# Kernel tuning notes

Measured on AMD Instinct MI355X. Metric: run time of the kernel, lower is better.

## Reference

```python
import jax, jax.numpy as jnp
import numpy as np
import math

B, D, NSTEPS = 16384, 256, 5
TEMP, ALPHA, ALPHA_A, ETA, EPS = 2.0, 0.2, 0.5, 1.0e4, 1e-10


def setup_inputs() -> dict:
    key = jax.random.key(0)
    ks = jax.random.split(key, 7)
    x = jax.random.bernoulli(ks[0], 0.5, (B, D)).astype(jnp.float32)  # binary state
    x_a = jax.random.normal(ks[1], (B, D), jnp.float32)  # auxiliary (continuous)
    A = jax.random.normal(ks[2], (D, D), jnp.float32)
    W = 0.1 * (A + A.T) / math.sqrt(D)  # symmetric coupling of quadratic EBM
    b = 0.1 * jax.random.normal(ks[3], (D,), jnp.float32)
    rr = jax.random.uniform(ks[4], (NSTEPS, B, D), jnp.float32)  # flip uniforms
    noise = jax.random.normal(ks[5], (NSTEPS, B, D), jnp.float32)  # Langevin noise
    accept_u = jax.random.uniform(ks[6], (NSTEPS, B), jnp.float32)  # MH uniforms
    return {"x": x, "x_a": x_a, "W": W, "b": b, "rr": rr, "noise": noise, "accept_u": accept_u}


def reference(x, x_a, W, b, rr, noise, accept_u):
    term2 = 1.0 / (2.0 * ALPHA)

    def energy(z):  # model(z): quadratic EBM, [B]
        return 0.5 * jnp.einsum('bd,de,be->b', z, W, z) + z @ b

    def diff_fn(z):  # approx_difference_function / temp: grad_E(z) * -(2z-1) / temp
        return (z @ W + b) * -(2.0 * z - 1.0) / TEMP

    def agrad(z, za):  # auxillary_gradient_function(eta, z, za)
        return (z - za) / ETA

    def step(carry, inp):
        x_cur, x_a_cur = carry
        rr_i, noise_i, u_i = inp
        ga = agrad(x_cur, x_a_cur)
        gm = diff_fn(x_cur) - ga / TEMP * -(2.0 * x_cur - 1.0)
        # exp(t)/(exp(t)+1) == sigmoid(t)
        flip_prob = jax.nn.sigmoid(gm - term2)
        ind = (rr_i < flip_prob).astype(x_cur.dtype)
        x_delta = (1.0 - x_cur) * ind + x_cur * (1.0 - ind)
        x_delta_a = x_a_cur + 0.5 * ALPHA_A * ga + math.sqrt(ALPHA_A) * noise_i
        lp_forward = jnp.sum(jnp.log(flip_prob * ind + (1.0 - flip_prob) * (1.0 - ind) + EPS), axis=-1)
        ga2 = agrad(x_delta, x_delta_a)
        gm2 = diff_fn(x_delta) - ga2 / TEMP * -(2.0 * x_delta - 1.0)
        fp2 = jax.nn.sigmoid(gm2 - term2)
        lp_reverse = jnp.sum(jnp.log(fp2 * ind + (1.0 - fp2) * (1.0 - ind) + EPS), axis=-1)
        m_term = (energy(x_delta) - jnp.sum((x_delta - x_delta_a) ** 2, axis=1) / (2.0 * ETA)) \
               - (energy(x_cur) - jnp.sum((x_cur - x_a_cur) ** 2, axis=1) / (2.0 * ETA))
        add_rev = jnp.sum((x_a_cur - (x_delta_a + 0.5 * ALPHA_A * ga2)) ** 2, axis=1) / (-2.0 * ALPHA_A)
        add_fwd = jnp.sum((x_delta_a - (x_a_cur + 0.5 * ALPHA_A * ga)) ** 2, axis=1) / (-2.0 * ALPHA_A)
        la = m_term + add_rev - add_fwd + lp_reverse - lp_forward
        # exp(la) > u  <=>  la > log(u); avoids overflow of exp
        a = (la > jnp.log(u_i)).astype(x_cur.dtype)
        x_new = x_delta * a[:, None] + x_cur * (1.0 - a[:, None])
        xa_new = x_delta_a * a[:, None] + x_a_cur * (1.0 - a[:, None])
        return (x_new, xa_new), None

    (x_out, xa_out), _ = jax.lax.scan(step, (x, x_a), (rr, noise, accept_u))
    return x_out, xa_out
```

## Files before the change

### kernel.cpp

```cpp
#include <hip/hip_runtime.h>
#include <math.h>


namespace {

constexpr int kB = 16384;
constexpr int kD = 256;
constexpr int kSteps = 5;

typedef float v2f __attribute__((ext_vector_type(2)));
typedef float v4f __attribute__((ext_vector_type(4)));

__device__ __forceinline__ v4f nt_load4(const float* p) {
  return __builtin_nontemporal_load(reinterpret_cast<const v4f*>(p));
}
__device__ __forceinline__ void nt_store4(float* p, v4f v) {
  __builtin_nontemporal_store(v, reinterpret_cast<v4f*>(p));
}

__device__ __forceinline__ float wave_sum(float v) {
#pragma unroll
  for (int off = 32; off > 0; off >>= 1) v += __shfl_xor(v, off, 64);
  return v;
}

__device__ __forceinline__ float sigmoid_f(float t) {
  if (t >= 0.0f) {
    float e = expf(-t);
    return 1.0f / (1.0f + e);
  } else {
    float e = expf(t);
    return e / (1.0f + e);
  }
}

__global__ __launch_bounds__(256) void els_fused(
    const float* __restrict__ x_in, const float* __restrict__ xa_in,
    const float* __restrict__ W, const float* __restrict__ bvec,
    const float* __restrict__ rr, const float* __restrict__ noise,
    const float* __restrict__ accept_u, float* __restrict__ out) {
  const int lane = threadIdx.x & 63;
  const int row = blockIdx.x * 4 + (threadIdx.x >> 6);
  const int c0 = lane << 2;

  const v4f x4 = nt_load4(x_in + (size_t)row * kD + c0);
  const v4f a4 = nt_load4(xa_in + (size_t)row * kD + c0);
  const float4 b4 = *reinterpret_cast<const float4*>(bvec + c0);
  float xv[4] = {x4.x, x4.y, x4.z, x4.w};
  float xa[4] = {a4.x, a4.y, a4.z, a4.w};
  const float bv[4] = {b4.x, b4.y, b4.z, b4.w};
  v2f y01 = {0.0f, 0.0f}, y23 = {0.0f, 0.0f};

  v4f r4 = nt_load4(rr + (size_t)row * kD + c0);
  v4f n4 = nt_load4(noise + (size_t)row * kD + c0);
  float u = accept_u[row];

#pragma unroll
  for (int i = 0; i < 4; ++i) {
    unsigned long long m = __ballot(xv[i] > 0.5f);
    const int cnt = __popcll(m);
    int t = 0;
    for (; t + 8 <= cnt; t += 8) {
      int j[8];
#pragma unroll
      for (int q = 0; q < 8; ++q) { j[q] = __builtin_ctzll(m); m &= m - 1; }
      float4 w[8];
#pragma unroll
      for (int q = 0; q < 8; ++q)
        w[q] = *reinterpret_cast<const float4*>(W + (size_t)(4 * j[q] + i) * kD + c0);
#pragma unroll
      for (int q = 0; q < 8; ++q) {
        y01 += (v2f){w[q].x, w[q].y};
        y23 += (v2f){w[q].z, w[q].w};
      }
    }
    for (; t < cnt; ++t) {
      const int jj = __builtin_ctzll(m); m &= m - 1;
      const float4 w = *reinterpret_cast<const float4*>(W + (size_t)(4 * jj + i) * kD + c0);
      y01 += (v2f){w.x, w.y};
      y23 += (v2f){w.z, w.w};
    }
  }

  for (int step = 0; step < kSteps; ++step) {
    const float rrv[4] = {r4.x, r4.y, r4.z, r4.w};
    const float nzv[4] = {n4.x, n4.y, n4.z, n4.w};
    const float ucur = u;

    const int sn = (step + 1 < kSteps) ? step + 1 : step;
    const size_t offn = ((size_t)sn * kB + row) * kD + c0;
    r4 = nt_load4(rr + offn);
    n4 = nt_load4(noise + offn);
    u = accept_u[(size_t)sn * kB + row];

    const float yv[4] = {y01.x, y01.y, y23.x, y23.y};
    float ga[4], xd[4], xda[4];
    bool ind[4];
    float s_lpf = 0.f, s_xy = 0.f, s_xb = 0.f, s_sqc = 0.f, s_fwd = 0.f;
    unsigned long long fm[4], sm[4];

#pragma unroll
    for (int i = 0; i < 4; ++i) {
      ga[i] = (xv[i] - xa[i]) / 1.0e4f;
      const float sgn = 1.0f - 2.0f * xv[i];
      const float gm = (yv[i] + bv[i] - ga[i]) * sgn / 2.0f;
      const float p = sigmoid_f(gm - 2.5f);
      ind[i] = rrv[i] < p;
      xd[i] = ind[i] ? 1.0f - xv[i] : xv[i];
      xda[i] = xa[i] + 0.25f * ga[i] + 0.70710678118654752f * nzv[i];
      const float pr = ind[i] ? p : 1.0f - p;
      s_lpf += logf(pr + 1e-10f);
      s_xy += xv[i] * yv[i];
      s_xb += xv[i] * bv[i];
      const float dc = xv[i] - xa[i];
      s_sqc += dc * dc;
      const float fw = xda[i] - (xa[i] + 0.25f * ga[i]);
      s_fwd += fw * fw;
      fm[i] = __ballot(ind[i]);
      sm[i] = __ballot(xv[i] > 0.5f);
    }

    v2f y2lo = y01, y2hi = y23;
#pragma unroll
    for (int i = 0; i < 4; ++i) {
      unsigned long long m = fm[i];
      const int cnt = __popcll(m);
      int t = 0;
      for (; t + 4 <= cnt; t += 4) {
        int j[4];
#pragma unroll
        for (int q = 0; q < 4; ++q) { j[q] = __builtin_ctzll(m); m &= m - 1; }
        float4 w[4];
        float s[4];
#pragma unroll
        for (int q = 0; q < 4; ++q) {
          s[q] = ((sm[i] >> j[q]) & 1ull) ? -1.0f : 1.0f;
          w[q] = *reinterpret_cast<const float4*>(W + (size_t)(4 * j[q] + i) * kD + c0);
        }
#pragma unroll
        for (int q = 0; q < 4; ++q) {
          const v2f sv = {s[q], s[q]};
          y2lo = __builtin_elementwise_fma(sv, (v2f){w[q].x, w[q].y}, y2lo);
          y2hi = __builtin_elementwise_fma(sv, (v2f){w[q].z, w[q].w}, y2hi);
        }
      }
      for (; t < cnt; ++t) {
        const int jj = __builtin_ctzll(m); m &= m - 1;
        const float s = ((sm[i] >> jj) & 1ull) ? -1.0f : 1.0f;
        const float4 w = *reinterpret_cast<const float4*>(W + (size_t)(4 * jj + i) * kD + c0);
        const v2f sv = {s, s};
        y2lo = __builtin_elementwise_fma(sv, (v2f){w.x, w.y}, y2lo);
        y2hi = __builtin_elementwise_fma(sv, (v2f){w.z, w.w}, y2hi);
      }
    }

    const float y2v[4] = {y2lo.x, y2lo.y, y2hi.x, y2hi.y};
    float s_lpr = 0.f, s_xdy = 0.f, s_xdb = 0.f, s_sqn = 0.f, s_rev = 0.f;
#pragma unroll
    for (int i = 0; i < 4; ++i) {
      const float ga2 = (xd[i] - xda[i]) / 1.0e4f;
      const float sgn2 = 1.0f - 2.0f * xd[i];
      const float gm2 = (y2v[i] + bv[i] - ga2) * sgn2 / 2.0f;
      const float p2 = sigmoid_f(gm2 - 2.5f);
      const float pr2 = ind[i] ? p2 : 1.0f - p2;
      s_lpr += logf(pr2 + 1e-10f);
      s_xdy += xd[i] * y2v[i];
      s_xdb += xd[i] * bv[i];
      const float dn = xd[i] - xda[i];
      s_sqn += dn * dn;
      const float rv = xa[i] - (xda[i] + 0.25f * ga2);
      s_rev += rv * rv;
    }

    s_lpf = wave_sum(s_lpf);
    s_lpr = wave_sum(s_lpr);
    s_xy = wave_sum(s_xy);
    s_xb = wave_sum(s_xb);
    s_xdy = wave_sum(s_xdy);
    s_xdb = wave_sum(s_xdb);
    s_sqc = wave_sum(s_sqc);
    s_sqn = wave_sum(s_sqn);
    s_rev = wave_sum(s_rev);
    s_fwd = wave_sum(s_fwd);

    const float E_cur = 0.5f * s_xy + s_xb;
    const float E_new = 0.5f * s_xdy + s_xdb;
    const float m_term = (E_new - s_sqn / 2.0e4f) - (E_cur - s_sqc / 2.0e4f);
    const float la = m_term - s_rev + s_fwd + s_lpr - s_lpf;
    const bool acc = la > logf(ucur);

#pragma unroll
    for (int i = 0; i < 4; ++i) {
      xv[i] = acc ? xd[i] : xv[i];
      xa[i] = acc ? xda[i] : xa[i];
    }
    y01 = acc ? y2lo : y01;
    y23 = acc ? y2hi : y23;
  }

  const v4f ox = {xv[0], xv[1], xv[2], xv[3]};
  const v4f oa = {xa[0], xa[1], xa[2], xa[3]};
  nt_store4(out + (size_t)row * kD + c0, ox);
  nt_store4(out + (size_t)kB * kD + (size_t)row * kD + c0, oa);
}

}

extern "C" void kernel_launch(void* const* d_in, const int* in_sizes, int n_in,
                              void* d_out, int out_size, void* d_ws, size_t ws_size,
                              hipStream_t stream) {
  const float* x = (const float*)d_in[0];
  const float* xa = (const float*)d_in[1];
  const float* W = (const float*)d_in[2];
  const float* b = (const float*)d_in[3];
  const float* rr = (const float*)d_in[4];
  const float* noise = (const float*)d_in[5];
  const float* au = (const float*)d_in[6];
  float* out = (float*)d_out;

  dim3 grid(kB / 4);
  dim3 block(256);
  hipLaunchKernelGGL(els_fused, grid, block, 0, stream, x, xa, W, b, rr, noise,
                     au, out);
}
```

Measured before the change: 382.4 us.

## Merge per-column bitmask loops into unified 8-wide W-row gather batches

Replaces the four per-column-slot gather loops, each with its own remainder tail, by a single stream that walks all four ballot masks in turn and fetches W rows in batches of eight. Exhausted slots are padded with row 0 and a zero weight. The first batch of the flip-delta gather is issued before the forward log-prob and energy reductions, so its load latency can overlap that arithmetic. The sigmoid is also made branchless. The cost is up to seven wasted padded loads per gather and more sequential branching in the mask extraction.

```diff
diff --git a/kernel.cpp b/kernel.cpp
--- a/kernel.cpp
+++ b/kernel.cpp
@@ -25,12 +25,46 @@
 }
 
 __device__ __forceinline__ float sigmoid_f(float t) {
-  if (t >= 0.0f) {
-    float e = expf(-t);
-    return 1.0f / (1.0f + e);
-  } else {
-    float e = expf(t);
-    return e / (1.0f + e);
+  const float e = expf(-fabsf(t));
+  const float num = (t >= 0.0f) ? 1.0f : e;
+  return num / (1.0f + e);
+}
+
+template <bool SIGNED>
+__device__ __forceinline__ void extract8(
+    unsigned long long& m0, unsigned long long& m1,
+    unsigned long long& m2, unsigned long long& m3,
+    const unsigned long long* smk, int* dq, float* sq) {
+#pragma unroll
+  for (int q = 0; q < 8; ++q) {
+    int d = -1;
+    if (m0) { const int j = __builtin_ctzll(m0); m0 &= m0 - 1; d = 4 * j; }
+    else if (m1) { const int j = __builtin_ctzll(m1); m1 &= m1 - 1; d = 4 * j + 1; }
+    else if (m2) { const int j = __builtin_ctzll(m2); m2 &= m2 - 1; d = 4 * j + 2; }
+    else if (m3) { const int j = __builtin_ctzll(m3); m3 &= m3 - 1; d = 4 * j + 3; }
+    if (d >= 0) {
+      sq[q] = SIGNED ? ((((smk[d & 3] >> (d >> 2)) & 1ull) ? -1.0f : 1.0f)) : 1.0f;
+      dq[q] = d;
+    } else {
+      dq[q] = 0;
+      sq[q] = 0.0f;
+    }
+  }
+}
+
+__device__ __forceinline__ void load8(const float* Wlane, const int* dq, float4* w) {
+#pragma unroll
+  for (int q = 0; q < 8; ++q)
+    w[q] = *reinterpret_cast<const float4*>(Wlane + (size_t)dq[q] * kD);
+}
+
+__device__ __forceinline__ void acc8(const float4* w, const float* sq,
+                                     v2f& ylo, v2f& yhi) {
+#pragma unroll
+  for (int q = 0; q < 8; ++q) {
+    const v2f sv = {sq[q], sq[q]};
+    ylo = __builtin_elementwise_fma(sv, (v2f){w[q].x, w[q].y}, ylo);
+    yhi = __builtin_elementwise_fma(sv, (v2f){w[q].z, w[q].w}, yhi);
   }
 }
 
@@ -42,6 +76,7 @@
   const int lane = threadIdx.x & 63;
   const int row = blockIdx.x * 4 + (threadIdx.x >> 6);
   const int c0 = lane << 2;
+  const float* Wl = W + c0;
 
   const v4f x4 = nt_load4(x_in + (size_t)row * kD + c0);
   const v4f a4 = nt_load4(xa_in + (size_t)row * kD + c0);
@@ -55,30 +90,18 @@
   v4f n4 = nt_load4(noise + (size_t)row * kD + c0);
   float u = accept_u[row];
 
-#pragma unroll
-  for (int i = 0; i < 4; ++i) {
-    unsigned long long m = __ballot(xv[i] > 0.5f);
-    const int cnt = __popcll(m);
-    int t = 0;
-    for (; t + 8 <= cnt; t += 8) {
-      int j[8];
-#pragma unroll
-      for (int q = 0; q < 8; ++q) { j[q] = __builtin_ctzll(m); m &= m - 1; }
-      float4 w[8];
-#pragma unroll
-      for (int q = 0; q < 8; ++q)
-        w[q] = *reinterpret_cast<const float4*>(W + (size_t)(4 * j[q] + i) * kD + c0);
-#pragma unroll
-      for (int q = 0; q < 8; ++q) {
-        y01 += (v2f){w[q].x, w[q].y};
-        y23 += (v2f){w[q].z, w[q].w};
-      }
-    }
-    for (; t < cnt; ++t) {
-      const int jj = __builtin_ctzll(m); m &= m - 1;
-      const float4 w = *reinterpret_cast<const float4*>(W + (size_t)(4 * jj + i) * kD + c0);
-      y01 += (v2f){w.x, w.y};
-      y23 += (v2f){w.z, w.w};
+  {
+    unsigned long long m0 = __ballot(xv[0] > 0.5f);
+    unsigned long long m1 = __ballot(xv[1] > 0.5f);
+    unsigned long long m2 = __ballot(xv[2] > 0.5f);
+    unsigned long long m3 = __ballot(xv[3] > 0.5f);
+    int rem = __popcll(m0) + __popcll(m1) + __popcll(m2) + __popcll(m3);
+    while (rem > 0) {
+      int dq[8]; float sq[8]; float4 w[8];
+      extract8<false>(m0, m1, m2, m3, nullptr, dq, sq);
+      load8(Wl, dq, w);
+      acc8(w, sq, y01, y23);
+      rem -= 8;
     }
   }
 
@@ -94,21 +117,34 @@
     u = accept_u[(size_t)sn * kB + row];
 
     const float yv[4] = {y01.x, y01.y, y23.x, y23.y};
-    float ga[4], xd[4], xda[4];
+
+    float ga[4], p[4];
     bool ind[4];
-    float s_lpf = 0.f, s_xy = 0.f, s_xb = 0.f, s_sqc = 0.f, s_fwd = 0.f;
     unsigned long long fm[4], sm[4];
-
 #pragma unroll
     for (int i = 0; i < 4; ++i) {
       ga[i] = (xv[i] - xa[i]) / 1.0e4f;
       const float sgn = 1.0f - 2.0f * xv[i];
       const float gm = (yv[i] + bv[i] - ga[i]) * sgn / 2.0f;
-      const float p = sigmoid_f(gm - 2.5f);
-      ind[i] = rrv[i] < p;
+      p[i] = sigmoid_f(gm - 2.5f);
+      ind[i] = rrv[i] < p[i];
+      fm[i] = __ballot(ind[i]);
+      sm[i] = __ballot(xv[i] > 0.5f);
+    }
+
+    unsigned long long g0 = fm[0], g1 = fm[1], g2 = fm[2], g3 = fm[3];
+    int rem = __popcll(g0) + __popcll(g1) + __popcll(g2) + __popcll(g3);
+    int dq[8]; float sq[8]; float4 w[8];
+    extract8<true>(g0, g1, g2, g3, sm, dq, sq);
+    load8(Wl, dq, w);
+
+    float xd[4], xda[4];
+    float s_lpf = 0.f, s_xy = 0.f, s_xb = 0.f, s_sqc = 0.f, s_fwd = 0.f;
+#pragma unroll
+    for (int i = 0; i < 4; ++i) {
       xd[i] = ind[i] ? 1.0f - xv[i] : xv[i];
       xda[i] = xa[i] + 0.25f * ga[i] + 0.70710678118654752f * nzv[i];
-      const float pr = ind[i] ? p : 1.0f - p;
+      const float pr = ind[i] ? p[i] : 1.0f - p[i];
       s_lpf += logf(pr + 1e-10f);
       s_xy += xv[i] * yv[i];
       s_xb += xv[i] * bv[i];
@@ -116,42 +152,16 @@
       s_sqc += dc * dc;
       const float fw = xda[i] - (xa[i] + 0.25f * ga[i]);
       s_fwd += fw * fw;
-      fm[i] = __ballot(ind[i]);
-      sm[i] = __ballot(xv[i] > 0.5f);
     }
 
     v2f y2lo = y01, y2hi = y23;
-#pragma unroll
-    for (int i = 0; i < 4; ++i) {
-      unsigned long long m = fm[i];
-      const int cnt = __popcll(m);
-      int t = 0;
-      for (; t + 4 <= cnt; t += 4) {
-        int j[4];
-#pragma unroll
-        for (int q = 0; q < 4; ++q) { j[q] = __builtin_ctzll(m); m &= m - 1; }
-        float4 w[4];
-        float s[4];
-#pragma unroll
-        for (int q = 0; q < 4; ++q) {
-          s[q] = ((sm[i] >> j[q]) & 1ull) ? -1.0f : 1.0f;
-          w[q] = *reinterpret_cast<const float4*>(W + (size_t)(4 * j[q] + i) * kD + c0);
-        }
-#pragma unroll
-        for (int q = 0; q < 4; ++q) {
-          const v2f sv = {s[q], s[q]};
-          y2lo = __builtin_elementwise_fma(sv, (v2f){w[q].x, w[q].y}, y2lo);
-          y2hi = __builtin_elementwise_fma(sv, (v2f){w[q].z, w[q].w}, y2hi);
-        }
-      }
-      for (; t < cnt; ++t) {
-        const int jj = __builtin_ctzll(m); m &= m - 1;
-        const float s = ((sm[i] >> jj) & 1ull) ? -1.0f : 1.0f;
-        const float4 w = *reinterpret_cast<const float4*>(W + (size_t)(4 * jj + i) * kD + c0);
-        const v2f sv = {s, s};
-        y2lo = __builtin_elementwise_fma(sv, (v2f){w.x, w.y}, y2lo);
-        y2hi = __builtin_elementwise_fma(sv, (v2f){w.z, w.w}, y2hi);
-      }
+    acc8(w, sq, y2lo, y2hi);
+    rem -= 8;
+    while (rem > 0) {
+      extract8<true>(g0, g1, g2, g3, sm, dq, sq);
+      load8(Wl, dq, w);
+      acc8(w, sq, y2lo, y2hi);
+      rem -= 8;
     }
 
     const float y2v[4] = {y2lo.x, y2lo.y, y2hi.x, y2hi.y};
```

Measured after the change: 409.2 us. +7.0%, slower.
